# Performance work log

Hardware: AMD Instinct MI355X
Metric: run time of the kernel (lower is better)

The kernel has to match this reference:

```python
import jax, jax.numpy as jnp
import numpy as np


def _hadamard(n: int) -> np.ndarray:
    # Sylvester construction; n must be a power of 2 (asserted in the torch source).
    H = np.array([[1.0]], dtype=np.float32)
    while H.shape[0] < n:
        H = np.block([[H, H], [H, -H]])
    return (H * (n ** -0.5)).astype(np.float32)


def _rotate_activation(x):
    # hadamard_transform(x, scale=D**-0.5) over the last dim; bf16 in/out like the CUDA kernel.
    D = x.shape[-1]
    H = jnp.asarray(_hadamard(D))
    return (x.astype(jnp.float32) @ H).astype(x.dtype)


def _cu_seqlen_kv_bounds(seq_lens, num_ctx_tokens):
    # Vectorized equivalent of compute_cu_seqlen_kv_bounds_nocache (repeat_interleave -> searchsorted).
    offsets = jnp.concatenate([jnp.zeros(1, jnp.int32), jnp.cumsum(seq_lens).astype(jnp.int32)])
    pos = jnp.arange(num_ctx_tokens, dtype=jnp.int32)
    batch_ids = jnp.searchsorted(offsets, pos, side='right').astype(jnp.int32) - 1
    ks = offsets[batch_ids]                 # start of this token's sequence in packed KV
    ke = ks + (pos - ks) + 1                # causal: local_position + 1 past the start
    return ks, ke


def setup_inputs() -> dict:
    key = jax.random.key(0)
    k1, k2, k3 = jax.random.split(key, 3)
    T, H, D = 2048, 16, 128
    q = jax.random.normal(k1, (T, H, D), dtype=jnp.bfloat16)
    k = jax.random.normal(k2, (T, D), dtype=jnp.bfloat16)
    weights = jax.random.uniform(k3, (T, H), dtype=jnp.float32) * (H ** -0.5)
    seq_lens = jnp.array([1024, 1024], dtype=jnp.int32)
    return {"q": q, "k": k, "weights": weights, "seq_lens": seq_lens, "index_topk": 256}


def reference(q, k, weights, seq_lens, index_topk):
    T = q.shape[0]
    # Hadamard-rotate q and k (lightning indexer activation rotation).
    qr = _rotate_activation(q).astype(jnp.float32)   # [T, H, D]
    kr = _rotate_activation(k).astype(jnp.float32)   # [T, D]
    # Index score: I[t, s] = sum_h w[t, h] * relu(q[t, h] . k[s])
    logits = jnp.einsum('thd,sd->ths', qr, kr)       # [T, H, T]
    scores = jnp.einsum('ths,th->ts', jax.nn.relu(logits), weights)  # [T, T]
    # Causal ragged-batch KV window per token.
    ks, ke = _cu_seqlen_kv_bounds(seq_lens, T)
    pos = jnp.arange(T, dtype=jnp.int32)
    valid = (pos[None, :] >= ks[:, None]) & (pos[None, :] < ke[:, None])
    NEG = jnp.float32(-1e30)
    masked = jnp.where(valid, scores, NEG)
    topk_vals, topk_idx = jax.lax.top_k(masked, index_topk)  # [T, topk]
    return topk_vals, topk_idx
```

## Files before the change

### kernel.cpp

```cpp
#include <hip/hip_runtime.h>
#include <hip/hip_bf16.h>
#include <stdint.h>

typedef __attribute__((ext_vector_type(8))) short short8;
typedef __attribute__((ext_vector_type(4))) float float4_t;
typedef __attribute__((ext_vector_type(16))) float float16_t;

#define DDIM 128
#define SORTN 256
#define LROW 136
#define SCAP 1088
#define NCHT 17

__device__ inline unsigned short f32_to_bf16_rne(float f) {
    uint32_t u = __float_as_uint(f);
    return (unsigned short)((u + 0x7FFFu + ((u >> 16) & 1u)) >> 16);
}
__device__ inline float bf16_to_f32(unsigned short h) {
    return __uint_as_float(((uint32_t)h) << 16);
}
__device__ inline int ks_of(const int* seq_lens, int n_seq, int t) {
    int off = 0, r = 0;
    for (int i = 0; i < n_seq; ++i) {
        int nx = off + seq_lens[i];
        if (t < nx) { r = off; break; }
        off = nx;
    }
    return r;
}

__global__ __launch_bounds__(256) void rotate_k_kernel(
        const unsigned short* __restrict__ k, unsigned short* __restrict__ kr, int T) {
    int row = blockIdx.x * 16 + (threadIdx.x >> 4);
    if (row >= T) return;
    int l16 = threadIdx.x & 15;
    short8 in = *(const short8*)(k + (size_t)row * DDIM + 8 * l16);
    float f[8];
    #pragma unroll
    for (int j = 0; j < 8; ++j) f[j] = bf16_to_f32((unsigned short)in[j]);
    #pragma unroll
    for (int b = 1; b <= 4; b <<= 1)
        #pragma unroll
        for (int j = 0; j < 8; ++j)
            if (!(j & b)) { float a = f[j], c = f[j | b]; f[j] = a + c; f[j | b] = a - c; }
    #pragma unroll
    for (int m = 1; m <= 8; m <<= 1) {
        bool hi = (l16 & m) != 0;
        #pragma unroll
        for (int j = 0; j < 8; ++j) {
            float o = __shfl_xor(f[j], m, 64);
            f[j] = hi ? (o - f[j]) : (f[j] + o);
        }
    }
    const float sc = 0.08838834764831845f;
    short8 out;
    #pragma unroll
    for (int j = 0; j < 8; ++j) out[j] = (short)f32_to_bf16_rne(f[j] * sc);
    *(short8*)(kr + (size_t)row * DDIM + 8 * l16) = out;
}

__global__ __launch_bounds__(256, 2) void fused_kernel(
        const unsigned short* __restrict__ q,
        const unsigned short* __restrict__ kr,
        const float* __restrict__ w,
        const int* __restrict__ seq_lens, int n_seq,
        float* __restrict__ out_vals, float* __restrict__ out_idx,
        int T, int H, int K, int Tt) {
    __shared__ __align__(16) unsigned short bL[128 * LROW];
    __shared__ __align__(16) float scw[4][SCAP];
    unsigned short* qst = (unsigned short*)&scw[0][0];

    const int tid  = threadIdx.x;
    const int wv   = tid >> 6, lane = tid & 63;
    const int col  = lane & 15, kgrp = lane >> 4;
    const int hi   = lane >> 5;
    const int l31  = lane & 31;
    const int srow = tid >> 4, sseg = tid & 15;

    const int m     = blockIdx.x;
    const int halfG = Tt >> 1;
    const int ttile = (Tt <= 1) ? 0 : ((m < halfG) ? m : (Tt - 1 - (m - halfG)));
    const int tt0   = ttile * 4;

    const int tg1 = tt0 + 1, tg2 = tt0 + 2, tg3 = tt0 + 3;
    const bool v0 = (tt0 < T), v1 = (tg1 < T), v2 = (tg2 < T), v3 = (tg3 < T);
    const int t0 = v0 ? tt0 : T - 1, t1 = v1 ? tg1 : T - 1;
    const int t2 = v2 ? tg2 : T - 1, t3 = v3 ? tg3 : T - 1;
    const int ks0 = ks_of(seq_lens, n_seq, t0);
    const int ks1 = ks_of(seq_lens, n_seq, t1);
    const int ks2 = ks_of(seq_lens, n_seq, t2);
    const int ks3 = ks_of(seq_lens, n_seq, t3);

    const int bks    = ks_of(seq_lens, n_seq, tt0);
    const int bke    = (tt0 + 4 < T) ? (tt0 + 4) : T;
    const int nchunk = (bke - bks + 127) >> 7;

    short8 pre[8];
    #pragma unroll
    for (int i = 0; i < 8; ++i) {
        int gs = bks + srow + 16 * i; if (gs > T - 1) gs = T - 1;
        pre[i] = *(const short8*)(kr + (size_t)gs * DDIM + sseg * 8);
    }

    const int t_r = (tt0 + wv < T) ? (tt0 + wv) : (T - 1);
    float f[4][8];
    const unsigned short* qrow = q + ((size_t)t_r * H + col) * DDIM + kgrp * 8;
    #pragma unroll
    for (int kk = 0; kk < 4; ++kk) {
        short8 v = *(const short8*)(qrow + kk * 32);
        #pragma unroll
        for (int j = 0; j < 8; ++j) f[kk][j] = bf16_to_f32((unsigned short)v[j]);
    }
    #pragma unroll
    for (int b = 1; b <= 4; b <<= 1)
        #pragma unroll
        for (int kk = 0; kk < 4; ++kk)
            #pragma unroll
            for (int j = 0; j < 8; ++j)
                if (!(j & b)) { float a = f[kk][j], c = f[kk][j | b];
                                f[kk][j] = a + c; f[kk][j | b] = a - c; }
    #pragma unroll
    for (int kk = 0; kk < 4; ++kk)
        #pragma unroll
        for (int j = 0; j < 8; ++j) {
            float o = __shfl_xor(f[kk][j], 16, 64);
            f[kk][j] = (kgrp & 1) ? (o - f[kk][j]) : (f[kk][j] + o);
        }
    #pragma unroll
    for (int kk = 0; kk < 4; ++kk)
        #pragma unroll
        for (int j = 0; j < 8; ++j) {
            float o = __shfl_xor(f[kk][j], 32, 64);
            f[kk][j] = (kgrp & 2) ? (o - f[kk][j]) : (f[kk][j] + o);
        }
    #pragma unroll
    for (int j = 0; j < 8; ++j) {
        { float a = f[0][j], c = f[1][j]; f[0][j] = a + c; f[1][j] = a - c; }
        { float a = f[2][j], c = f[3][j]; f[2][j] = a + c; f[3][j] = a - c; }
        { float a = f[0][j], c = f[2][j]; f[0][j] = a + c; f[2][j] = a - c; }
        { float a = f[1][j], c = f[3][j]; f[1][j] = a + c; f[3][j] = a - c; }
    }
    const float scl = 0.08838834764831845f;
    #pragma unroll
    for (int kk = 0; kk < 4; ++kk) {
        short8 o;
        #pragma unroll
        for (int j = 0; j < 8; ++j) o[j] = (short)f32_to_bf16_rne(f[kk][j] * scl);
        *(short8*)&qst[(wv * 16 + col) * LROW + kgrp * 8 + kk * 32] = o;
    }
    __syncthreads();

    short8 afrag0[8], afrag1[8];
    {
        const unsigned short* qr0 = qst + l31 * LROW + hi * 8;
        const unsigned short* qr1 = qst + (32 + l31) * LROW + hi * 8;
        #pragma unroll
        for (int k8 = 0; k8 < 8; ++k8) {
            afrag0[k8] = *(const short8*)(qr0 + 16 * k8);
            afrag1[k8] = *(const short8*)(qr1 + 16 * k8);
        }
    }
    float w0r[8], w1r[8], w2r[8], w3r[8];
    #pragma unroll
    for (int r = 0; r < 8; ++r) {
        int h = (r & 3) + 8 * ((r >> 2) & 1) + 4 * hi;
        w0r[r] = w[(size_t)t0 * H + h];
        w1r[r] = w[(size_t)t1 * H + h];
        w2r[r] = w[(size_t)t2 * H + h];
        w3r[r] = w[(size_t)t3 * H + h];
    }
    __syncthreads();

    const int nrow = wv * 32 + l31;
    for (int c = 0; c < nchunk; ++c) {
        const int kv0 = bks + (c << 7);
        #pragma unroll
        for (int i = 0; i < 8; ++i)
            *(short8*)&bL[(srow + 16 * i) * LROW + sseg * 8] = pre[i];
        __syncthreads();
        if (c + 1 < nchunk) {
            int kvn = kv0 + 128;
            #pragma unroll
            for (int i = 0; i < 8; ++i) {
                int gs = kvn + srow + 16 * i; if (gs > T - 1) gs = T - 1;
                pre[i] = *(const short8*)(kr + (size_t)gs * DDIM + sseg * 8);
            }
        }
        const unsigned short* brow = &bL[nrow * LROW + hi * 8];
        float16_t acc01 = {0.f, 0.f, 0.f, 0.f, 0.f, 0.f, 0.f, 0.f,
                           0.f, 0.f, 0.f, 0.f, 0.f, 0.f, 0.f, 0.f};
        float16_t acc23 = {0.f, 0.f, 0.f, 0.f, 0.f, 0.f, 0.f, 0.f,
                           0.f, 0.f, 0.f, 0.f, 0.f, 0.f, 0.f, 0.f};
        __builtin_amdgcn_s_setprio(1);
        #pragma unroll
        for (int k8 = 0; k8 < 8; ++k8) {
            short8 bf = *(const short8*)(brow + 16 * k8);
            acc01 = __builtin_amdgcn_mfma_f32_32x32x16_bf16(afrag0[k8], bf, acc01, 0, 0, 0);
            acc23 = __builtin_amdgcn_mfma_f32_32x32x16_bf16(afrag1[k8], bf, acc23, 0, 0, 0);
        }
        __builtin_amdgcn_s_setprio(0);
        float p0 = 0.f, p1 = 0.f, p2 = 0.f, p3 = 0.f;
        #pragma unroll
        for (int r = 0; r < 8; ++r) {
            float a = acc01[r];     a = a > 0.f ? a : 0.f; p0 += w0r[r] * a;
            float b = acc01[r + 8]; b = b > 0.f ? b : 0.f; p1 += w1r[r] * b;
            float g = acc23[r];     g = g > 0.f ? g : 0.f; p2 += w2r[r] * g;
            float d = acc23[r + 8]; d = d > 0.f ? d : 0.f; p3 += w3r[r] * d;
        }
        p0 += __shfl_xor(p0, 32, 64);
        p1 += __shfl_xor(p1, 32, 64);
        p2 += __shfl_xor(p2, 32, 64);
        p3 += __shfl_xor(p3, 32, 64);
        const int s = kv0 + nrow;
        if (hi == 0) {
            if (v0 && s >= ks0 && s <= t0) scw[0][s - ks0] = p0;
            if (v2 && s >= ks2 && s <= t2) scw[2][s - ks2] = p2;
        } else {
            if (v1 && s >= ks1 && s <= t1) scw[1][s - ks1] = p1;
            if (v3 && s >= ks3 && s <= t3) scw[3][s - ks3] = p3;
        }
        __syncthreads();
    }

    const int t_s = tt0 + wv;
    if (t_s >= T) return;
    const int ks_w = ks_of(seq_lens, n_seq, t_s);
    const int ke_w = t_s + 1;
    const int n    = ke_w - ks_w;

    const int nch = (n + 63) >> 6;
    uint32_t ukey[NCHT];
    #pragma unroll
    for (int c = 0; c < NCHT; ++c) {
        if (c < nch) {
            int i = c * 64 + lane;
            ukey[c] = (i < n) ? __float_as_uint(scw[wv][i]) : 0u;
        } else ukey[c] = 0u;
    }
    unsigned long long* candw = (unsigned long long*)&scw[wv][0];

    const int Keff = (n < K) ? n : K;
    uint32_t ustar = 0;
    int ttake = K;
    if (n > K) {
        uint32_t lo = 0, hia = 0x80000000u;
        for (int it = 0; it < 31; ++it) {
            uint32_t mid = (lo + hia) >> 1;
            int total = 0;
            #pragma unroll
            for (int c = 0; c < NCHT; ++c)
                if (c < nch) total += (int)__popcll(__ballot(ukey[c] >= mid));
            if (total >= K) lo = mid; else hia = mid;
        }
        ustar = lo;
        int tg = 0;
        #pragma unroll
        for (int c = 0; c < NCHT; ++c)
            if (c < nch) tg += (int)__popcll(__ballot(ukey[c] > ustar));
        ttake = K - tg;
    }

    {
        const unsigned long long ltm = (1ull << lane) - 1ull;
        int base = 0, tieBase = 0;
        const bool selAll = (n <= K);
        #pragma unroll
        for (int c = 0; c < NCHT; ++c) {
            if (c < nch) {
                int i = c * 64 + lane;
                bool inb = (i < n);
                uint32_t u = ukey[c];
                bool isGt  = inb && (selAll || u > ustar);
                bool isTie = inb && !selAll && (u == ustar);
                unsigned long long mt = __ballot(isTie);
                int tr = tieBase + (int)__popcll(mt & ltm);
                bool take = isGt || (isTie && tr < ttake);
                unsigned long long mk = __ballot(take);
                if (take) {
                    int pos = base + (int)__popcll(mk & ltm);
                    int s = ks_w + i;
                    if (pos < SORTN)
                        candw[pos] = ((((unsigned long long)u << 11) |
                                       (unsigned long long)(T - 1 - s)) + 1ull);
                }
                base    += (int)__popcll(mk);
                tieBase += (int)__popcll(mt);
            }
        }
        for (int i = Keff + lane; i < SORTN; i += 64) candw[i] = 0ull;
    }

    unsigned long long kreg[4];
    #pragma unroll
    for (int r = 0; r < 4; ++r) kreg[r] = candw[4 * lane + r];

    #define CX(a, b, dsc) { unsigned long long _mx = (a) > (b) ? (a) : (b); \
                            unsigned long long _mn = (a) > (b) ? (b) : (a); \
                            (a) = (dsc) ? _mx : _mn; (b) = (dsc) ? _mn : _mx; }
    #pragma unroll
    for (int size = 2; size <= SORTN; size <<= 1) {
        #pragma unroll
        for (int stride = SORTN >> 1; stride >= 4; stride >>= 1) {
            if (stride > (size >> 1)) continue;
            int lmask = stride >> 2;
            #pragma unroll
            for (int r = 0; r < 4; ++r) {
                int e = 4 * lane + r;
                unsigned long long other = __shfl_xor(kreg[r], lmask, 64);
                bool desc = ((e & size) == 0);
                bool iAmLow = ((e & stride) == 0);
                bool keepMax = (iAmLow == desc);
                kreg[r] = keepMax ? (kreg[r] > other ? kreg[r] : other)
                                  : (kreg[r] < other ? kreg[r] : other);
            }
        }
        if (size >= 4) {
            bool d = (((4 * lane) & size) == 0);
            CX(kreg[0], kreg[2], d);
            CX(kreg[1], kreg[3], d);
            CX(kreg[0], kreg[1], d);
            CX(kreg[2], kreg[3], d);
        } else {
            CX(kreg[0], kreg[1], true);
            CX(kreg[2], kreg[3], false);
        }
    }
    #undef CX

    if (4 * lane < K) {
        float4_t v4, i4;
        #pragma unroll
        for (int r = 0; r < 4; ++r) {
            int e = 4 * lane + r;
            unsigned long long key = kreg[r];
            float v; int idx;
            if (key != 0ull) {
                unsigned long long km1 = key - 1ull;
                v = __uint_as_float((uint32_t)(km1 >> 11));
                idx = T - 1 - (int)(km1 & 0x7FFull);
            } else {
                int pidx = e - Keff;
                idx = (pidx < ks_w) ? pidx : (ke_w + (pidx - ks_w));
                v = -1e30f;
            }
            v4[r] = v; i4[r] = (float)idx;
        }
        *(float4_t*)(out_vals + (size_t)t_s * K + 4 * lane) = v4;
        *(float4_t*)(out_idx  + (size_t)t_s * K + 4 * lane) = i4;
    }
}

extern "C" void kernel_launch(void* const* d_in, const int* in_sizes, int n_in,
                              void* d_out, int out_size, void* d_ws, size_t ws_size,
                              hipStream_t stream) {
    const unsigned short* q = (const unsigned short*)d_in[0];
    const unsigned short* k = (const unsigned short*)d_in[1];
    const float* w          = (const float*)d_in[2];
    const int* seq_lens     = (const int*)d_in[3];
    const int n_seq = in_sizes[3];
    const int T = in_sizes[1] / DDIM;
    const int H = in_sizes[2] / T;
    const int K = out_size / (2 * T);

    unsigned short* kr = (unsigned short*)d_ws;
    float* out_vals = (float*)d_out;
    float* out_idx  = out_vals + (size_t)T * K;

    rotate_k_kernel<<<dim3((T + 15) / 16), dim3(256), 0, stream>>>(k, kr, T);
    const int Tt = (T + 3) / 4;
    fused_kernel<<<dim3(Tt), dim3(256), 0, stream>>>(
        q, kr, w, seq_lens, n_seq, out_vals, out_idx, T, H, K, Tt);
}
```

Baseline: 105.5 us.

## Load K fragments directly into registers, drop LDS staging and per-chunk barriers

Each wave now loads its MFMA B-operand fragments for K straight from global memory into registers, double-buffered across two register sets, instead of staging 128-row K chunks through shared memory. This removes the LDS write/read round trip and two __syncthreads per chunk, and frees the 34KB bL buffer, which may allow higher occupancy. The cost is more global traffic, since each lane reads its own row slices with less coalescing, and higher register pressure from 16 short8 buffers.

```diff
diff --git a/kernel.cpp b/kernel.cpp
--- a/kernel.cpp
+++ b/kernel.cpp
@@ -66,7 +66,6 @@
         const int* __restrict__ seq_lens, int n_seq,
         float* __restrict__ out_vals, float* __restrict__ out_idx,
         int T, int H, int K, int Tt) {
-    __shared__ __align__(16) unsigned short bL[128 * LROW];
     __shared__ __align__(16) float scw[4][SCAP];
     unsigned short* qst = (unsigned short*)&scw[0][0];
 
@@ -75,7 +74,6 @@
     const int col  = lane & 15, kgrp = lane >> 4;
     const int hi   = lane >> 5;
     const int l31  = lane & 31;
-    const int srow = tid >> 4, sseg = tid & 15;
 
     const int m     = blockIdx.x;
     const int halfG = Tt >> 1;
@@ -95,12 +93,17 @@
     const int bke    = (tt0 + 4 < T) ? (tt0 + 4) : T;
     const int nchunk = (bke - bks + 127) >> 7;
 
-    short8 pre[8];
-    #pragma unroll
-    for (int i = 0; i < 8; ++i) {
-        int gs = bks + srow + 16 * i; if (gs > T - 1) gs = T - 1;
-        pre[i] = *(const short8*)(kr + (size_t)gs * DDIM + sseg * 8);
-    }
+    const int nrow = wv * 32 + l31;
+
+    auto load_chunk = [&](short8* dst, int kv0) {
+        int gr = kv0 + nrow; if (gr > T - 1) gr = T - 1;
+        const unsigned short* base = kr + (size_t)gr * DDIM + hi * 8;
+        #pragma unroll
+        for (int k8 = 0; k8 < 8; ++k8) dst[k8] = *(const short8*)(base + 16 * k8);
+    };
+
+    short8 bA[8], bB[8];
+    load_chunk(bA, bks);
 
     const int t_r = (tt0 + wv < T) ? (tt0 + wv) : (T - 1);
     float f[4][8];
@@ -171,22 +174,7 @@
     }
     __syncthreads();
 
-    const int nrow = wv * 32 + l31;
-    for (int c = 0; c < nchunk; ++c) {
-        const int kv0 = bks + (c << 7);
-        #pragma unroll
-        for (int i = 0; i < 8; ++i)
-            *(short8*)&bL[(srow + 16 * i) * LROW + sseg * 8] = pre[i];
-        __syncthreads();
-        if (c + 1 < nchunk) {
-            int kvn = kv0 + 128;
-            #pragma unroll
-            for (int i = 0; i < 8; ++i) {
-                int gs = kvn + srow + 16 * i; if (gs > T - 1) gs = T - 1;
-                pre[i] = *(const short8*)(kr + (size_t)gs * DDIM + sseg * 8);
-            }
-        }
-        const unsigned short* brow = &bL[nrow * LROW + hi * 8];
+    auto compute_chunk = [&](const short8* bf, int kv0) {
         float16_t acc01 = {0.f, 0.f, 0.f, 0.f, 0.f, 0.f, 0.f, 0.f,
                            0.f, 0.f, 0.f, 0.f, 0.f, 0.f, 0.f, 0.f};
         float16_t acc23 = {0.f, 0.f, 0.f, 0.f, 0.f, 0.f, 0.f, 0.f,
@@ -194,9 +182,8 @@
         __builtin_amdgcn_s_setprio(1);
         #pragma unroll
         for (int k8 = 0; k8 < 8; ++k8) {
-            short8 bf = *(const short8*)(brow + 16 * k8);
-            acc01 = __builtin_amdgcn_mfma_f32_32x32x16_bf16(afrag0[k8], bf, acc01, 0, 0, 0);
-            acc23 = __builtin_amdgcn_mfma_f32_32x32x16_bf16(afrag1[k8], bf, acc23, 0, 0, 0);
+            acc01 = __builtin_amdgcn_mfma_f32_32x32x16_bf16(afrag0[k8], bf[k8], acc01, 0, 0, 0);
+            acc23 = __builtin_amdgcn_mfma_f32_32x32x16_bf16(afrag1[k8], bf[k8], acc23, 0, 0, 0);
         }
         __builtin_amdgcn_s_setprio(0);
         float p0 = 0.f, p1 = 0.f, p2 = 0.f, p3 = 0.f;
@@ -219,8 +206,17 @@
             if (v1 && s >= ks1 && s <= t1) scw[1][s - ks1] = p1;
             if (v3 && s >= ks3 && s <= t3) scw[3][s - ks3] = p3;
         }
-        __syncthreads();
-    }
+    };
+
+    for (int c = 0; c < nchunk; c += 2) {
+        if (c + 1 < nchunk) load_chunk(bB, bks + ((c + 1) << 7));
+        compute_chunk(bA, bks + (c << 7));
+        if (c + 1 < nchunk) {
+            if (c + 2 < nchunk) load_chunk(bA, bks + ((c + 2) << 7));
+            compute_chunk(bB, bks + ((c + 1) << 7));
+        }
+    }
+    __syncthreads();
 
     const int t_s = tt0 + wv;
     if (t_s >= T) return;
```

Measured after the change: 102.8 us. 1.03x faster.
